# Kernel tuning notes

Measured on AMD Instinct MI355X. Metric: run time of the kernel, lower is better.

Reference implementation:

```python
import jax, jax.numpy as jnp
import numpy as np

B, T, C, H = 4, 2048, 1024, 16
D = C // H  # head_dim = 64
ROPE_BASE = 10000.0
EPS = 1e-6


def _rms_norm(x):
    return x / jnp.sqrt(jnp.mean(x * x, axis=-1, keepdims=True) + EPS)


def _rope_tables(t_len, d, dtype):
    inv_freq = 1.0 / (ROPE_BASE ** (jnp.arange(0, d, 2, dtype=jnp.float32) / d))
    t = jnp.arange(t_len, dtype=jnp.float32)
    freqs = jnp.outer(t, inv_freq)  # [T, D/2]
    return jnp.cos(freqs).astype(dtype)[None, None], jnp.sin(freqs).astype(dtype)[None, None]


def _apply_rotary(x, cos, sin):
    d = x.shape[-1] // 2
    x1, x2 = x[..., :d], x[..., d:]
    return jnp.concatenate([x1 * cos + x2 * sin, -x1 * sin + x2 * cos], axis=-1)


def setup_inputs() -> dict:
    key = jax.random.key(0)
    k1, k2, k3, k4, k5 = jax.random.split(key, 5)
    x = jax.random.normal(k1, (B, T, C), dtype=jnp.float32)
    Wqkv = jax.random.normal(k2, (C, 3 * C), dtype=jnp.float32) * 0.02
    bqkv = jax.random.normal(k3, (3 * C,), dtype=jnp.float32) * 0.02
    # NOTE: original zero-inits c_proj.weight; randomized here for a non-trivial baseline.
    Wproj = jax.random.normal(k4, (C, C), dtype=jnp.float32) * 0.02
    bproj = jax.random.normal(k5, (C,), dtype=jnp.float32) * 0.02
    lamb = jnp.float32(0.5)
    return {"x": x, "Wqkv": Wqkv, "bqkv": bqkv, "Wproj": Wproj, "bproj": bproj, "lamb": lamb}


def reference(x, Wqkv, bqkv, Wproj, bproj, lamb):
    b, t, c = x.shape
    qkv = x @ Wqkv + bqkv  # [B,T,3C]
    q, k, v = jnp.split(qkv, 3, axis=-1)
    # [B,T,C] -> [B,H,T,D]
    to_heads = lambda z: z.reshape(b, t, H, D).transpose(0, 2, 1, 3)
    query, key_, value = to_heads(q), to_heads(k), to_heads(v)
    # v1 defaults to value -> blend is identity, kept for faithfulness
    value = (1.0 - lamb) * value + lamb * value
    query = _rms_norm(query)
    key_ = _rms_norm(key_)
    cos, sin = _rope_tables(t, D, x.dtype)
    query = _apply_rotary(query, cos, sin)
    key_ = _apply_rotary(key_, cos, sin)
    # causal SDPA
    scale = 1.0 / jnp.sqrt(jnp.float32(D)).astype(x.dtype)
    scores = jnp.einsum('bhqd,bhkd->bhqk', query, key_) * scale
    causal = jnp.tril(jnp.ones((t, t), dtype=bool))
    scores = jnp.where(causal[None, None], scores, jnp.finfo(scores.dtype).min)
    probs = jax.nn.softmax(scores, axis=-1)
    attn = jnp.einsum('bhqk,bhkd->bhqd', probs, value)
    attn = attn.transpose(0, 2, 1, 3).reshape(b, t, c)
    out = attn @ Wproj + bproj
    return out, value
```

## Files before the change

### kernel.cpp

```cpp
#include <hip/hip_runtime.h>
#include <math.h>

#define B_   4
#define T_   2048
#define C_   1024
#define H_   16
#define D_   64
#define TC3  3072

typedef __attribute__((ext_vector_type(8))) short short8;
typedef __attribute__((ext_vector_type(4))) short short4b;
typedef __attribute__((ext_vector_type(8))) unsigned short ushortv8;
typedef __attribute__((ext_vector_type(4))) float f32x4;
typedef __attribute__((ext_vector_type(4))) __bf16 bf16x4;

__device__ __forceinline__ float bf2f(unsigned short u) {
  unsigned int x = ((unsigned int)u) << 16;
  float f; __builtin_memcpy(&f, &x, 4); return f;
}
__device__ __forceinline__ unsigned short f2bf(float f) {
  unsigned int x; __builtin_memcpy(&x, &f, 4);
  x += 0x7fff + ((x >> 16) & 1);
  return (unsigned short)(x >> 16);
}

#define MFMA32(a, b, c) __builtin_amdgcn_mfma_f32_16x16x32_bf16(a, b, c, 0, 0, 0)
#if __has_builtin(__builtin_amdgcn_mfma_f32_16x16x16_bf16)
#define MFMA16(a, b, c) __builtin_amdgcn_mfma_f32_16x16x16_bf16(a, b, c, 0, 0, 0)
#else
#define MFMA16(a, b, c) __builtin_amdgcn_mfma_f32_16x16x16bf16_1k(a, b, c, 0, 0, 0)
#endif

#define GLOAD_LDS(gp, lp) __builtin_amdgcn_global_load_lds( \
    (const __attribute__((address_space(1))) unsigned int*)(gp), \
    (__attribute__((address_space(3))) unsigned int*)(lp), 16, 0, 0)

__global__ __launch_bounds__(256)
void convert_bf16(const float* __restrict__ x, unsigned short* __restrict__ xb) {
  const size_t i = ((size_t)blockIdx.x * 256 + threadIdx.x) * 8;
  float4 f0 = *(const float4*)(x + i);
  float4 f1 = *(const float4*)(x + i + 4);
  ushortv8 u = { f2bf(f0.x), f2bf(f0.y), f2bf(f0.z), f2bf(f0.w),
                 f2bf(f1.x), f2bf(f1.y), f2bf(f1.z), f2bf(f1.w) };
  *(ushortv8*)(xb + i) = u;
}

__global__ __launch_bounds__(256)
void transpose_bf16(const float* __restrict__ W, unsigned short* __restrict__ WT,
                    int K, int N) {
  __shared__ float tile[64][65];
  const int k0 = blockIdx.y * 64, n0 = blockIdx.x * 64;
  const int r = threadIdx.x >> 4, c4 = (threadIdx.x & 15) * 4;
#pragma unroll
  for (int p = 0; p < 4; ++p) {
    int kk = p * 16 + r;
    float4 v = *(const float4*)(W + (size_t)(k0 + kk) * N + n0 + c4);
    tile[kk][c4 + 0] = v.x; tile[kk][c4 + 1] = v.y;
    tile[kk][c4 + 2] = v.z; tile[kk][c4 + 3] = v.w;
  }
  __syncthreads();
#pragma unroll
  for (int p = 0; p < 4; ++p) {
    int nn = p * 16 + r;
    ushort4 o = { f2bf(tile[c4 + 0][nn]), f2bf(tile[c4 + 1][nn]),
                  f2bf(tile[c4 + 2][nn]), f2bf(tile[c4 + 3][nn]) };
    *(ushort4*)(WT + (size_t)(n0 + nn) * K + k0 + c4) = o;
  }
}

template<bool OUT_BF16>
__global__ __launch_bounds__(256)
void gemm_mfma(const unsigned short* __restrict__ Ab,
               const unsigned short* __restrict__ Bt,
               const float* __restrict__ bias, void* __restrict__ Cv,
               int K, int lda, int ldb, int ldc) {
  __shared__ unsigned short As[128 * 64];
  __shared__ unsigned short Bs[128 * 64];
  const int tid = threadIdx.x;
  const int l = tid & 63, w = tid >> 6;
  const int m0 = blockIdx.y * 128, n0 = blockIdx.x * 128;
  const int wm = (w & 1) * 64, wn = (w >> 1) * 64;
  const int fr = l & 15, g = l >> 4;

  f32x4 acc[4][4];
#pragma unroll
  for (int i = 0; i < 4; ++i)
#pragma unroll
    for (int j = 0; j < 4; ++j) acc[i][j] = (f32x4)0.f;

  const int gr = l >> 3;
  const int gc = (l & 7) ^ gr;

  for (int kt = 0; kt < K; kt += 64) {
    __syncthreads();
#pragma unroll
    for (int q = 0; q < 4; ++q) {
      int rr = (w * 4 + q) * 8 + gr;
      GLOAD_LDS(Ab + (size_t)(m0 + rr) * lda + kt + gc * 8,
                &As[(w * 4 + q) * 512]);
      GLOAD_LDS(Bt + (size_t)(n0 + rr) * ldb + kt + gc * 8,
                &Bs[(w * 4 + q) * 512]);
    }
    __syncthreads();

#pragma unroll
    for (int s = 0; s < 2; ++s) {
      const int cofs = (((s * 4 + g) ^ (fr & 7)) << 3);
      short8 a[4], b[4];
#pragma unroll
      for (int i = 0; i < 4; ++i)
        a[i] = *(const short8*)&As[(wm + i * 16 + fr) * 64 + cofs];
#pragma unroll
      for (int j = 0; j < 4; ++j)
        b[j] = *(const short8*)&Bs[(wn + j * 16 + fr) * 64 + cofs];
#pragma unroll
      for (int i = 0; i < 4; ++i)
#pragma unroll
        for (int j = 0; j < 4; ++j)
          acc[i][j] = MFMA32(a[i], b[j], acc[i][j]);
    }
  }

#pragma unroll
  for (int j = 0; j < 4; ++j) {
    const int n = n0 + wn + j * 16 + fr;
    const float bv = bias[n];
#pragma unroll
    for (int i = 0; i < 4; ++i) {
#pragma unroll
      for (int rg = 0; rg < 4; ++rg) {
        const int m = m0 + wm + i * 16 + g * 4 + rg;
        float v = acc[i][j][rg] + bv;
        if (OUT_BF16) ((unsigned short*)Cv)[(size_t)m * ldc + n] = f2bf(v);
        else          ((float*)Cv)[(size_t)m * ldc + n] = v;
      }
    }
  }
}

__global__ __launch_bounds__(256)
void rmsrope_kernel(unsigned short* __restrict__ qkv) {
  const int unit = blockIdx.x * 4 + (threadIdx.x >> 6);
  const int lane = threadIdx.x & 63;
  const int b = unit / (T_ * H_);
  const int rem = unit % (T_ * H_);
  const int t = rem / H_;
  const int h = rem % H_;
  const size_t base = (size_t)(b * T_ + t) * TC3;

  const int i = lane & 31;
  const float inv = __builtin_amdgcn_exp2f(-13.2877123795494f * (float)(2 * i)
                                           * (1.0f / 64.0f));
  const float ang = (float)t * inv;
  const float cs = cosf(ang);
  const float sn = sinf(ang);

  {
    const size_t idx = base + h * 64 + lane;
    float q = bf2f(qkv[idx]);
    float ss = q * q;
    ss += __shfl_xor(ss, 32); ss += __shfl_xor(ss, 16);
    ss += __shfl_xor(ss, 8);  ss += __shfl_xor(ss, 4);
    ss += __shfl_xor(ss, 2);  ss += __shfl_xor(ss, 1);
    float qn = q * (1.0f / sqrtf(ss * (1.0f / 64.0f) + 1e-6f));
    float part = __shfl_xor(qn, 32);
    float out = (lane < 32) ? (qn * cs + part * sn) : (qn * cs - part * sn);
    qkv[idx] = f2bf(out);
  }
  {
    const size_t idx = base + C_ + h * 64 + lane;
    float k = bf2f(qkv[idx]);
    float ss = k * k;
    ss += __shfl_xor(ss, 32); ss += __shfl_xor(ss, 16);
    ss += __shfl_xor(ss, 8);  ss += __shfl_xor(ss, 4);
    ss += __shfl_xor(ss, 2);  ss += __shfl_xor(ss, 1);
    float kn = k * (1.0f / sqrtf(ss * (1.0f / 64.0f) + 1e-6f));
    float part = __shfl_xor(kn, 32);
    float out = (lane < 32) ? (kn * cs + part * sn) : (kn * cs - part * sn);
    qkv[idx] = f2bf(out);
  }
}

__global__ __launch_bounds__(256)
void vtrans_kernel(const unsigned short* __restrict__ qkv,
                   const float* __restrict__ lambp,
                   unsigned short* __restrict__ vT,
                   float* __restrict__ valOut) {
  __shared__ float tile[64][65];
  const int t0 = blockIdx.x * 64;
  const int head = blockIdx.y;
  const int b = head >> 4, h = head & 15;
  const float lamb = lambp[0];
  const int r = threadIdx.x >> 4, c4 = (threadIdx.x & 15) * 4;
#pragma unroll
  for (int p = 0; p < 4; ++p) {
    int tt = p * 16 + r;
    ushort4 raw = *(const ushort4*)(
        qkv + (size_t)(b * T_ + t0 + tt) * TC3 + 2 * C_ + h * 64 + c4);
    float4 f;
    f.x = (1.f - lamb) * bf2f(raw.x) + lamb * bf2f(raw.x);
    f.y = (1.f - lamb) * bf2f(raw.y) + lamb * bf2f(raw.y);
    f.z = (1.f - lamb) * bf2f(raw.z) + lamb * bf2f(raw.z);
    f.w = (1.f - lamb) * bf2f(raw.w) + lamb * bf2f(raw.w);
    tile[tt][c4 + 0] = f.x; tile[tt][c4 + 1] = f.y;
    tile[tt][c4 + 2] = f.z; tile[tt][c4 + 3] = f.w;
    *(float4*)(valOut + ((size_t)head * T_ + t0 + tt) * D_ + c4) = f;
  }
  __syncthreads();
#pragma unroll
  for (int p = 0; p < 4; ++p) {
    int d = p * 16 + r;
    ushort4 o = { f2bf(tile[c4 + 0][d]), f2bf(tile[c4 + 1][d]),
                  f2bf(tile[c4 + 2][d]), f2bf(tile[c4 + 3][d]) };
    *(ushort4*)(vT + ((size_t)head * D_ + d) * T_ + t0 + c4) = o;
  }
}

#define SCL_ (0.125f * 1.44269504088896f)

__device__ __forceinline__ void attn_tile(
    const unsigned short* __restrict__ Ks,
    const unsigned short* __restrict__ Vs,
    const short8 (&qf)[2][2], int qrow0 , int k0,
    int fr, int quad, int f8,
    float (&l_pt)[2], f32x4 (&o)[2][4]) {
  f32x4 st[2][4];
#pragma unroll
  for (int i = 0; i < 2; ++i)
#pragma unroll
    for (int j = 0; j < 4; ++j) st[i][j] = (f32x4)0.f;

  __builtin_amdgcn_s_setprio(1);
#pragma unroll
  for (int kc = 0; kc < 2; ++kc) {
    const int cofs = (((kc * 4 + quad) ^ f8) << 3);
#pragma unroll
    for (int j = 0; j < 4; ++j) {
      short8 kf = *(const short8*)&Ks[(j * 16 + fr) * 64 + cofs];
      st[0][j] = MFMA32(kf, qf[kc][0], st[0][j]);
      st[1][j] = MFMA32(kf, qf[kc][1], st[1][j]);
    }
  }
  __builtin_amdgcn_s_setprio(0);

  short4b pa[2][4];
#pragma unroll
  for (int i = 0; i < 2; ++i) {
    const int qg = qrow0 + i * 16 + fr;
#pragma unroll
    for (int j = 0; j < 4; ++j) {
      const int kg = k0 + j * 16 + quad * 4;
#pragma unroll
      for (int r = 0; r < 4; ++r) {
        float arg = st[i][j][r] * SCL_;
        if (kg + r > qg) arg = -INFINITY;
        float p = __builtin_amdgcn_exp2f(arg);
        l_pt[i] += p;
        st[i][j][r] = p;
      }
      bf16x4 pb = { (__bf16)st[i][j][0], (__bf16)st[i][j][1],
                    (__bf16)st[i][j][2], (__bf16)st[i][j][3] };
      pa[i][j] = __builtin_bit_cast(short4b, pb);
    }
  }

  __builtin_amdgcn_s_setprio(1);
#pragma unroll
  for (int c = 0; c < 4; ++c) {
    const int vofs = ((((c * 2 + (quad >> 1)) ^ f8) << 3) + (quad & 1) * 4);
#pragma unroll
    for (int jd = 0; jd < 4; ++jd) {
      short4b vf = *(const short4b*)&Vs[(jd * 16 + fr) * 64 + vofs];
      o[0][jd] = MFMA16(pa[0][c], vf, o[0][jd]);
      o[1][jd] = MFMA16(pa[1][c], vf, o[1][jd]);
    }
  }
  __builtin_amdgcn_s_setprio(0);
}

__device__ __forceinline__ void attn_store(
    unsigned short* __restrict__ qkv, int bT, int h, int qrow0,
    int fr, int quad, float (&l_pt)[2], f32x4 (&o)[2][4]) {
#pragma unroll
  for (int i = 0; i < 2; ++i) {
    float lv = l_pt[i];
    lv += __shfl_xor(lv, 16);
    lv += __shfl_xor(lv, 32);
    float inv = 1.0f / lv;
    float invq[4];
#pragma unroll
    for (int r = 0; r < 4; ++r) invq[r] = __shfl(inv, quad * 4 + r);
#pragma unroll
    for (int jd = 0; jd < 4; ++jd) {
      const int d = jd * 16 + fr;
#pragma unroll
      for (int r = 0; r < 4; ++r) {
        const int row = qrow0 + i * 16 + quad * 4 + r;
        qkv[(size_t)(bT + row) * TC3 + 2 * C_ + h * 64 + d] =
            f2bf(o[i][jd][r] * invq[r]);
      }
    }
  }
}

__global__ __launch_bounds__(256)
void flash_mfma(unsigned short* __restrict__ qkv,
                const unsigned short* __restrict__ vT) {
  __shared__ unsigned short Qs[128 * 64];
  __shared__ unsigned short Ks[64 * 64];
  __shared__ unsigned short Vs[64 * 64];

  const int z = blockIdx.z;
  const int xx = ((int)blockIdx.x + ((z >> 1) << 3)) & 15;
  const int qt = (z & 1) ? (15 - xx) : xx;
  const int b  = z;
  const int h  = blockIdx.y;
  const int bT = b * T_;

  const int tid = threadIdx.x;
  const int w = tid >> 6, l = tid & 63;
  const int fr = l & 15, quad = l >> 4;
  const int q0 = qt * 128;
  const int gr = l >> 3;
  const int gc = (l & 7) ^ gr;
  const int f8 = fr & 7;

#pragma unroll
  for (int s = 0; s < 4; ++s) {
    int row = w * 32 + s * 8 + gr;
    GLOAD_LDS(qkv + (size_t)(bT + q0 + row) * TC3 + h * 64 + gc * 8,
              &Qs[(w * 32 + s * 8) * 64]);
  }
  __syncthreads();

  short8 qf[2][2];
#pragma unroll
  for (int kc = 0; kc < 2; ++kc) {
    const int cofs = (((kc * 4 + quad) ^ f8) << 3);
    qf[kc][0] = *(const short8*)&Qs[(w * 32 + fr) * 64 + cofs];
    qf[kc][1] = *(const short8*)&Qs[(w * 32 + 16 + fr) * 64 + cofs];
  }

  float l_pt[2] = {0.f, 0.f};
  f32x4 o[2][4];
#pragma unroll
  for (int i = 0; i < 2; ++i)
#pragma unroll
    for (int j = 0; j < 4; ++j) o[i][j] = (f32x4)0.f;

  const int nk = 2 * qt + 2;
  const int qr0 = q0 + w * 32;

  for (int kt = 0; kt < nk; ++kt) {
    const int k0 = kt * 64;
    __syncthreads();
#pragma unroll
    for (int s = 0; s < 2; ++s) {
      int row = w * 16 + s * 8;
      GLOAD_LDS(qkv + (size_t)(bT + k0 + row + gr) * TC3 + C_ + h * 64 + gc * 8,
                &Ks[row * 64]);
      GLOAD_LDS(vT + ((size_t)(b * H_ + h) * D_ + row + gr) * T_ + k0 + gc * 8,
                &Vs[row * 64]);
    }
    __syncthreads();

    attn_tile(Ks, Vs, qf, qr0, k0, fr, quad, f8, l_pt, o);
  }

  attn_store(qkv, bT, h, qr0, fr, quad, l_pt, o);
}

extern "C" void kernel_launch(void* const* d_in, const int* in_sizes, int n_in,
                              void* d_out, int out_size, void* d_ws, size_t ws_size,
                              hipStream_t stream) {
  const float* x     = (const float*)d_in[0];
  const float* Wqkv  = (const float*)d_in[1];
  const float* bqkv  = (const float*)d_in[2];
  const float* Wproj = (const float*)d_in[3];
  const float* bproj = (const float*)d_in[4];
  const float* lamb  = (const float*)d_in[5];

  float* out     = (float*)d_out;
  float* val_out = out + (size_t)B_ * T_ * C_;

  unsigned short* qkvb   = (unsigned short*)d_ws;
  unsigned short* WqkvT  = qkvb + (size_t)B_ * T_ * TC3;
  unsigned short* WprojT = WqkvT + (size_t)TC3 * C_;
  unsigned short* vT     = WprojT + (size_t)C_ * C_;
  unsigned short* xb     = vT + (size_t)B_ * H_ * D_ * T_;

  convert_bf16<<<dim3((B_ * T_ * C_) / 2048), 256, 0, stream>>>(x, xb);
  transpose_bf16<<<dim3(TC3 / 64, C_ / 64), 256, 0, stream>>>(Wqkv, WqkvT, C_, TC3);
  transpose_bf16<<<dim3(C_ / 64, C_ / 64), 256, 0, stream>>>(Wproj, WprojT, C_, C_);

  gemm_mfma<true><<<dim3(TC3 / 128, (B_ * T_) / 128), 256, 0, stream>>>(
      xb, WqkvT, bqkv, qkvb, C_, C_, C_, TC3);

  rmsrope_kernel<<<dim3((B_ * T_ * H_) / 4), 256, 0, stream>>>(qkvb);

  vtrans_kernel<<<dim3(T_ / 64, B_ * H_), 256, 0, stream>>>(qkvb, lamb, vT, val_out);

  flash_mfma<<<dim3(16, H_, B_), 256, 0, stream>>>(qkvb, vT);

  gemm_mfma<false><<<dim3(C_ / 128, (B_ * T_) / 128), 256, 0, stream>>>(
      qkvb + 2 * C_, WprojT, bproj, out, C_, TC3, C_, C_);
}
```

Before: 318.5 us.

## Double-buffer K/V tiles in flash attention and alias Q staging into them

Replaces the single K/V shared-memory buffers with two ping-pong buffers so the async global-to-LDS load of the next tile overlaps the MFMA work on the current tile, with one combined waitcnt-plus-barrier per tile instead of two barriers. The Q staging buffer is removed and Q is loaded into the second buffer pair before being moved to registers, which keeps LDS usage the same. The loop is unrolled by two and relies on nk always being even. The custom sync waits for all outstanding memory ops, which may limit how much overlap is actually achieved.

```diff
diff --git a/kernel.cpp b/kernel.cpp
--- a/kernel.cpp
+++ b/kernel.cpp
@@ -218,6 +218,12 @@
 
 #define SCL_ (0.125f * 1.44269504088896f)
 
+#define PIPE_SYNC() do { \
+  asm volatile("s_waitcnt vmcnt(0) lgkmcnt(0)" ::: "memory"); \
+  __builtin_amdgcn_s_barrier(); \
+  asm volatile("" ::: "memory"); \
+} while (0)
+
 __device__ __forceinline__ void attn_tile(
     const unsigned short* __restrict__ Ks,
     const unsigned short* __restrict__ Vs,
@@ -306,9 +312,10 @@
 __global__ __launch_bounds__(256)
 void flash_mfma(unsigned short* __restrict__ qkv,
                 const unsigned short* __restrict__ vT) {
-  __shared__ unsigned short Qs[128 * 64];
-  __shared__ unsigned short Ks[64 * 64];
-  __shared__ unsigned short Vs[64 * 64];
+  __shared__ unsigned short Ks0[64 * 64];
+  __shared__ unsigned short Vs0[64 * 64];
+  __shared__ unsigned short Ks1[64 * 64];
+  __shared__ unsigned short Vs1[64 * 64];
 
   const int z = blockIdx.z;
   const int xx = ((int)blockIdx.x + ((z >> 1) << 3)) & 15;
@@ -325,21 +332,38 @@
   const int gc = (l & 7) ^ gr;
   const int f8 = fr & 7;
 
+#define STAGE(KS, VS, KT) do { \
+  const int _k0 = (KT) * 64; \
+  _Pragma("unroll") \
+  for (int s_ = 0; s_ < 2; ++s_) { \
+    int row_ = w * 16 + s_ * 8; \
+    GLOAD_LDS(qkv + (size_t)(bT + _k0 + row_ + gr) * TC3 + C_ + h * 64 + gc * 8, \
+              &KS[row_ * 64]); \
+    GLOAD_LDS(vT + ((size_t)(b * H_ + h) * D_ + row_ + gr) * T_ + _k0 + gc * 8, \
+              &VS[row_ * 64]); \
+  } \
+} while (0)
+
 #pragma unroll
   for (int s = 0; s < 4; ++s) {
-    int row = w * 32 + s * 8 + gr;
-    GLOAD_LDS(qkv + (size_t)(bT + q0 + row) * TC3 + h * 64 + gc * 8,
-              &Qs[(w * 32 + s * 8) * 64]);
-  }
+    int rbase = w * 32 + s * 8;
+    unsigned short* qdst = (rbase < 64) ? &Ks0[rbase * 64]
+                                        : &Vs0[(rbase - 64) * 64];
+    GLOAD_LDS(qkv + (size_t)(bT + q0 + rbase + gr) * TC3 + h * 64 + gc * 8, qdst);
+  }
+  STAGE(Ks1, Vs1, 0);
   __syncthreads();
 
+  const unsigned short* Qb = (w < 2) ? Ks0 : Vs0;
+  const int rq = (w < 2) ? w * 32 : (w - 2) * 32;
   short8 qf[2][2];
 #pragma unroll
   for (int kc = 0; kc < 2; ++kc) {
     const int cofs = (((kc * 4 + quad) ^ f8) << 3);
-    qf[kc][0] = *(const short8*)&Qs[(w * 32 + fr) * 64 + cofs];
-    qf[kc][1] = *(const short8*)&Qs[(w * 32 + 16 + fr) * 64 + cofs];
-  }
+    qf[kc][0] = *(const short8*)&Qb[(rq + fr) * 64 + cofs];
+    qf[kc][1] = *(const short8*)&Qb[(rq + 16 + fr) * 64 + cofs];
+  }
+  __syncthreads();
 
   float l_pt[2] = {0.f, 0.f};
   f32x4 o[2][4];
@@ -351,23 +375,17 @@
   const int nk = 2 * qt + 2;
   const int qr0 = q0 + w * 32;
 
-  for (int kt = 0; kt < nk; ++kt) {
-    const int k0 = kt * 64;
-    __syncthreads();
-#pragma unroll
-    for (int s = 0; s < 2; ++s) {
-      int row = w * 16 + s * 8;
-      GLOAD_LDS(qkv + (size_t)(bT + k0 + row + gr) * TC3 + C_ + h * 64 + gc * 8,
-                &Ks[row * 64]);
-      GLOAD_LDS(vT + ((size_t)(b * H_ + h) * D_ + row + gr) * T_ + k0 + gc * 8,
-                &Vs[row * 64]);
-    }
-    __syncthreads();
-
-    attn_tile(Ks, Vs, qf, qr0, k0, fr, quad, f8, l_pt, o);
+  for (int kt = 0; kt < nk; kt += 2) {
+    STAGE(Ks0, Vs0, kt + 1);
+    attn_tile(Ks1, Vs1, qf, qr0, kt * 64, fr, quad, f8, l_pt, o);
+    PIPE_SYNC();
+    if (kt + 2 < nk) STAGE(Ks1, Vs1, kt + 2);
+    attn_tile(Ks0, Vs0, qf, qr0, (kt + 1) * 64, fr, quad, f8, l_pt, o);
+    if (kt + 2 < nk) PIPE_SYNC();
   }
 
   attn_store(qkv, bT, h, qr0, fr, quad, l_pt, o);
+#undef STAGE
 }
 
 extern "C" void kernel_launch(void* const* d_in, const int* in_sizes, int n_in,
```

Measured after the change: 345.1 us. 8.4% more time.
